# Kernel optimization log

Hardware: AMD Instinct MI355X
Metric: run time of the kernel (lower is better)

The kernel has to match this reference:

```python
import jax, jax.numpy as jnp
import numpy as np

NEG = 0.01  # torch leaky_relu default slope


def conv1d(x, w, pad):
    # x: [B, C, L], w: [O, I, K], stride 1, no bias (as in FC-STGNN extractor)
    return jax.lax.conv_general_dilated(x, w, (1,), [(pad, pad)], dimension_numbers=('NCH', 'OIH', 'NCH'))


def maxpool2(x):
    # MaxPool1d(kernel=2, stride=2, padding=1); torch pads with -inf for max
    return jax.lax.reduce_window(x, -jnp.inf, jax.lax.max, (1, 1, 2), (1, 1, 2), ((0, 0), (0, 0), (1, 1)))


def pos_encoding(n, d):
    # standard sinusoidal PE table, rows 0..n-1 (n <= max_len=5000)
    pos = jnp.arange(n, dtype=jnp.float32)[:, None]
    div = jnp.exp(jnp.arange(0, d, 2, dtype=jnp.float32) * (-float(np.log(10000.0)) / d))
    pe = jnp.zeros((n, d), jnp.float32)
    pe = pe.at[:, 0::2].set(jnp.sin(pos * div))
    pe = pe.at[:, 1::2].set(jnp.cos(pos * div))
    return pe


def mpnn_block(x, gw, gb, bng, bnb, tw, tb):
    # GraphConvpoolMPNN_block_v6 with time_length=1, time_window_size=1, stride=1:
    # one window, decay mask = ones, mean-pool over the size-1 time window is identity.
    bs, two_h, N = x.shape
    X = x.reshape(bs, N, two_h)                                   # (bs*num_windows, num_node*tw, input_dim)
    h = X @ gw + gb                                               # Dot_Graph_Construction mapping
    adj = jnp.einsum('bnd,bmd->bnm', h, h)                        # dot-product adjacency
    eye = jnp.eye(N, dtype=X.dtype)
    adj = jax.nn.leaky_relu(adj - eye * 1e8, NEG)
    adj = jax.nn.softmax(adj, axis=-1) + eye
    Xb = X * bng + bnb                                            # BatchNorm1d eval (running mean 0 / var 1)
    out = jax.nn.leaky_relu(jnp.einsum('bnm,bmd->bnd', adj, Xb) @ tw + tb, NEG)  # MPNN_mk k=1
    return out                                                    # [bs, N, hidden]


def setup_inputs() -> dict:
    key = jax.random.key(0)
    ks = jax.random.split(key, 20)
    bs, D, N = 4, 128, 1024
    H, OUT, KS = 64, 32, 8        # lstmhidden_dim, lstmout_dim, conv_kernel
    HID = 64                      # hidden_dim
    TWOH = 2 * HID
    CONV_OUT = 18
    NCLS = 6
    f32 = jnp.float32
    rn = lambda k, s, sc: jax.random.normal(k, s, f32) * sc
    return {
        'x_enc': rn(ks[0], (bs, D, N), 1.0),
        'x_mark_enc': rn(ks[1], (bs, D, 4), 1.0),
        'x_dec': rn(ks[2], (bs, D // 2, N), 1.0),
        'x_mark_dec': rn(ks[3], (bs, D // 2, 4), 1.0),
        'conv_w1': rn(ks[4], (H, 1, KS), 1.0 / np.sqrt(KS)),
        'bn1_g': jnp.ones((H,), f32), 'bn1_b': jnp.zeros((H,), f32),
        'conv_w2': rn(ks[5], (2 * H, H, KS), 1.0 / np.sqrt(H * KS)),
        'bn2_g': jnp.ones((2 * H,), f32), 'bn2_b': jnp.zeros((2 * H,), f32),
        'conv_w3': rn(ks[6], (OUT, 2 * H, KS), 1.0 / np.sqrt(2 * H * KS)),
        'bn3_g': jnp.ones((OUT,), f32), 'bn3_b': jnp.zeros((OUT,), f32),
        'map2_w': rn(ks[7], (OUT * CONV_OUT, TWOH), 1.0 / np.sqrt(OUT * CONV_OUT)),
        'map2_b': jnp.zeros((TWOH,), f32),
        'map2_bn_g': jnp.ones((TWOH,), f32), 'map2_bn_b': jnp.zeros((TWOH,), f32),
        'g1_w': rn(ks[8], (TWOH, TWOH), 1.0 / np.sqrt(TWOH)), 'g1_b': jnp.zeros((TWOH,), f32),
        'm1_bn_g': jnp.ones((TWOH,), f32), 'm1_bn_b': jnp.zeros((TWOH,), f32),
        't1_w': rn(ks[9], (TWOH, HID), 1.0 / np.sqrt(TWOH)), 't1_b': jnp.zeros((HID,), f32),
        'g2_w': rn(ks[10], (TWOH, TWOH), 1.0 / np.sqrt(TWOH)), 'g2_b': jnp.zeros((TWOH,), f32),
        'm2_bn_g': jnp.ones((TWOH,), f32), 'm2_bn_b': jnp.zeros((TWOH,), f32),
        't2_w': rn(ks[11], (TWOH, HID), 1.0 / np.sqrt(TWOH)), 't2_b': jnp.zeros((HID,), f32),
        'fc1_w': rn(ks[12], (HID * 2 * N, TWOH), 1.0 / np.sqrt(HID * 2 * N)), 'fc1_b': jnp.zeros((TWOH,), f32),
        'fc2_w': rn(ks[13], (TWOH, TWOH), 1.0 / np.sqrt(TWOH)), 'fc2_b': jnp.zeros((TWOH,), f32),
        'fc3_w': rn(ks[14], (TWOH, HID), 1.0 / np.sqrt(TWOH)), 'fc3_b': jnp.zeros((HID,), f32),
        'fc4_w': rn(ks[15], (HID, NCLS), 1.0 / np.sqrt(HID)), 'fc4_b': jnp.zeros((NCLS,), f32),
    }


def reference(x_enc, x_mark_enc, x_dec, x_mark_dec,
              conv_w1, bn1_g, bn1_b, conv_w2, bn2_g, bn2_b, conv_w3, bn3_g, bn3_b,
              map2_w, map2_b, map2_bn_g, map2_bn_b,
              g1_w, g1_b, m1_bn_g, m1_bn_b, t1_w, t1_b,
              g2_w, g2_b, m2_bn_g, m2_bn_b, t2_w, t2_b,
              fc1_w, fc1_b, fc2_w, fc2_b, fc3_w, fc3_b, fc4_w, fc4_b):
    bs, D, N = x_enc.shape
    k = conv_w1.shape[-1]
    # nonlin_map: 1D-CNN feature extractor over each (sample, node) signal
    a = jnp.swapaxes(x_enc.reshape(bs * N, D, 1), 1, 2)           # [bs*N, 1, D]
    a = maxpool2(jax.nn.relu(conv1d(a, conv_w1, k // 2) * bn1_g[None, :, None] + bn1_b[None, :, None]))
    a = maxpool2(jax.nn.relu(conv1d(a, conv_w2, 4) * bn2_g[None, :, None] + bn2_b[None, :, None]))
    a = maxpool2(jax.nn.relu(conv1d(a, conv_w3, 4) * bn3_g[None, :, None] + bn3_b[None, :, None]))
    a = a.reshape(bs * N, -1)                                     # [bs*N, lstmout_dim*conv_out]
    # nonlin_map2: Linear + BatchNorm1d (eval mode affine)
    a = (a @ map2_w + map2_b) * map2_bn_g + map2_bn_b             # [bs*N, 2h]
    two_h = a.shape[-1]
    # positional encoding with the exact reshape/transpose traffic of the torch forward
    x = jnp.swapaxes(a.reshape(bs, N, two_h), 1, 2).reshape(bs * N, two_h)
    x = x + pos_encoding(bs * N, two_h)
    x = jnp.swapaxes(x.reshape(bs, N, two_h), 1, 2)               # [bs, 2h, N]
    # two graph MPNN branches
    o1 = mpnn_block(x, g1_w, g1_b, m1_bn_g, m1_bn_b, t1_w, t1_b)
    o2 = mpnn_block(x, g2_w, g2_b, m2_bn_g, m2_bn_b, t2_w, t2_b)
    f = jnp.concatenate([o1.reshape(bs, -1), o2.reshape(bs, -1)], axis=-1)
    # MLP head
    f = jax.nn.relu(f @ fc1_w + fc1_b)
    f = jax.nn.relu(f @ fc2_w + fc2_b)
    f = jax.nn.relu(f @ fc3_w + fc3_b)
    return f @ fc4_w + fc4_b                                      # [bs, n_class]
```

## Files before the change

### kernel.cpp

```cpp
#include <hip/hip_runtime.h>
#include <hip/hip_bf16.h>
#include <math.h>

#define NEG 0.01f
__device__ __forceinline__ float lrelu(float v){ return v > 0.f ? v : NEG*v; }
__device__ __forceinline__ float frelu(float v){ return v > 0.f ? v : 0.f; }

typedef __attribute__((ext_vector_type(8))) short bf16x8;
typedef __attribute__((ext_vector_type(4))) float f32x4;

__device__ __forceinline__ unsigned short f2bf(float x){
    unsigned int u = __float_as_uint(x);
    unsigned int r = (u + 0x7FFFu + ((u>>16)&1u)) >> 16;
    return (unsigned short)r;
}
__device__ __forceinline__ float bf2f(unsigned short h){
    return __uint_as_float(((unsigned int)h) << 16);
}
__device__ __forceinline__ unsigned short F2B(float x){
    __hip_bfloat16 h = __float2bfloat16(x);
    return *reinterpret_cast<unsigned short*>(&h);
}

__global__ __launch_bounds__(256) void k_prep(const float* __restrict__ w2, const float* __restrict__ w3,
    const float* __restrict__ m2w, const float* __restrict__ t1w, const float* __restrict__ t2w,
    unsigned short* __restrict__ w2s, unsigned short* __restrict__ w3s, unsigned short* __restrict__ m2wbT,
    unsigned short* __restrict__ twThi, unsigned short* __restrict__ twTlo)
{
    int gid = blockIdx.x*256 + threadIdx.x;
    if (gid < 73728) {
        int j = gid / 576, f = gid % 576;
        m2wbT[gid] = f2bf(m2w[f*128 + j]);
    }
    if (gid < 65536) {
        int jj = gid & 7, q = (gid>>3)&3, o = (gid>>5)&127, ks = (gid>>12)&1, k = gid>>13;
        int c = ks*32 + q*8 + jj;
        w2s[gid] = f2bf(w2[o*512 + c*8 + k]);
    }
    if (gid < 32768) {
        int jj = gid & 7, q = (gid>>3)&3, o = (gid>>5)&31, ks = (gid>>10)&3, k = gid>>12;
        int c = ks*32 + q*8 + jj;
        w3s[gid] = f2bf(w3[o*1024 + c*8 + k]);
    }
    if (gid < 16384) {
        int d = gid & 127, e = (gid>>7)&63, br = gid>>13;
        float x = (br ? t2w : t1w)[d*64 + e];
        unsigned short hh = f2bf(x);
        twThi[gid] = hh;
        twTlo[gid] = f2bf(x - bf2f(hh));
    }
}

__global__ __launch_bounds__(256) void k_conv(
    const float* __restrict__ xenc,
    const float* __restrict__ w1, const float* __restrict__ g1, const float* __restrict__ b1,
    const unsigned short* __restrict__ w2s, const float* __restrict__ g2, const float* __restrict__ b2,
    const unsigned short* __restrict__ w3s, const float* __restrict__ g3, const float* __restrict__ b3,
    unsigned short* __restrict__ aflatG)
{
    __shared__ __align__(16) unsigned char smraw[22208];
    float* sigp = (float*)smraw;
    unsigned short* p1T = (unsigned short*)(smraw + 576);
    unsigned short* p2T = (unsigned short*)(smraw + 10304);
    unsigned short* astage = (unsigned short*)(smraw + 21056);

    const int t = threadIdx.x;
    const int s = blockIdx.x;

    {
        unsigned int* zz = (unsigned int*)(smraw + 576);
        for (int i = t; i < 5120; i += 256) zz[i] = 0u;
        if (t < 144) sigp[t] = 0.f;
    }
    __syncthreads();
    if (t < 128) sigp[4 + t] = xenc[(size_t)s*128 + t];
    __syncthreads();

    {
        const int c = t & 63, qg = t >> 6;
        float wr[8];
        #pragma unroll
        for (int k = 0; k < 8; ++k) wr[k] = w1[c*8 + k];
        const float g = g1[c], b = b1[c];
        const int qs = qg*17;
        float win[9];
        {
            int base = 2*qs - 1;
            #pragma unroll
            for (int x = 0; x < 9; ++x) win[x] = (base + x >= 0) ? sigp[base + x] : 0.f;
        }
        #pragma unroll
        for (int j = 0; j < 17; ++j) {
            int q = qs + j;
            float s0 = 0.f, s1 = 0.f;
            #pragma unroll
            for (int k = 0; k < 8; ++k) { s0 += win[k]*wr[k]; s1 += win[k+1]*wr[k]; }
            float v = frelu(s1*g + b);
            if (q > 0) v = fmaxf(v, frelu(s0*g + b));
            if (q < 65) {
                int row = q + 4;
                p1T[row*64 + (((c>>3) ^ (row&7))<<3) + (c&7)] = F2B(v);
            }
            #pragma unroll
            for (int x = 0; x < 7; ++x) win[x] = win[x+2];
            win[7] = sigp[2*q + 8];
            win[8] = sigp[2*q + 9];
        }
    }
    __syncthreads();

    {
        const int wv = t >> 6, l = t & 63, lg = l >> 4, lr = l & 15;
        const int pbase = ((lr & 7) << 1) + (lr >> 3) - 1;
        f32x4 acc[2][5] = {};
        for (int k = 0; k < 8; ++k) {
            for (int ks = 0; ks < 2; ++ks) {
                bf16x8 af[2];
                #pragma unroll
                for (int oi = 0; oi < 2; ++oi) {
                    int o = (wv*2 + oi)*16 + lr;
                    af[oi] = *(const bf16x8*)(w2s + ((((k*2 + ks)*128 + o)*4 + lg)<<3));
                }
                const int q = ks*4 + lg;
                #pragma unroll
                for (int nt = 0; nt < 5; ++nt) {
                    int row = nt*16 + pbase + k; row = row > 75 ? 75 : row;
                    bf16x8 bfv = *(const bf16x8*)(p1T + row*64 + ((q ^ (row&7))<<3));
                    acc[0][nt] = __builtin_amdgcn_mfma_f32_16x16x32_bf16(af[0], bfv, acc[0][nt], 0,0,0);
                    acc[1][nt] = __builtin_amdgcn_mfma_f32_16x16x32_bf16(af[1], bfv, acc[1][nt], 0,0,0);
                }
            }
        }
        float ga[2][4], ba[2][4];
        #pragma unroll
        for (int oi = 0; oi < 2; ++oi)
            #pragma unroll
            for (int r = 0; r < 4; ++r) {
                int o = (wv*2 + oi)*16 + lg*4 + r;
                ga[oi][r] = g2[o]; ba[oi][r] = b2[o];
            }
        #pragma unroll
        for (int oi = 0; oi < 2; ++oi)
            #pragma unroll
            for (int nt = 0; nt < 5; ++nt) {
                int p = nt*16 + pbase;
                bool valid = (p >= 0) && (p <= 65);
                float vv[4];
                #pragma unroll
                for (int r = 0; r < 4; ++r) {
                    float v = frelu(acc[oi][nt][r]*ga[oi][r] + ba[oi][r]);
                    vv[r] = valid ? v : -3.0e38f;
                }
                float pv[4];
                #pragma unroll
                for (int r = 0; r < 4; ++r) pv[r] = fmaxf(vv[r], __shfl_xor(vv[r], 8));
                int q = nt*8 + (lr & 7);
                if ((lr >> 3) == 0 && q < 34) {
                    int row2 = q + 4;
                    int o0 = (wv*2 + oi)*16 + lg*4;
                    uint2 pk;
                    pk.x = (unsigned int)F2B(pv[0]) | ((unsigned int)F2B(pv[1]) << 16);
                    pk.y = (unsigned int)F2B(pv[2]) | ((unsigned int)F2B(pv[3]) << 16);
                    *(uint2*)&p2T[row2*128 + (((o0>>3) ^ (row2&15))<<3) + (o0&7)] = pk;
                }
            }
    }
    __syncthreads();

    {
        const int wv = t >> 6, l = t & 63, lg = l >> 4, lr = l & 15;
        const int ot = wv & 1, ntb = (wv >> 1) * 2;
        const int ncnt = (wv < 2) ? 2 : 1;
        const int pbase = ((lr & 7) << 1) + (lr >> 3) - 1;
        f32x4 acc[2] = {};
        for (int k = 0; k < 8; ++k) {
            for (int ks = 0; ks < 4; ++ks) {
                int o = ot*16 + lr;
                bf16x8 af = *(const bf16x8*)(w3s + ((((k*4 + ks)*32 + o)*4 + lg)<<3));
                const int q = ks*4 + lg;
                #pragma unroll
                for (int ni = 0; ni < 2; ++ni) {
                    if (ni < ncnt) {
                        int row = (ntb + ni)*16 + pbase + k; row = row > 41 ? 41 : row;
                        bf16x8 bfv = *(const bf16x8*)(p2T + row*128 + ((q ^ (row&15))<<3));
                        acc[ni] = __builtin_amdgcn_mfma_f32_16x16x32_bf16(af, bfv, acc[ni], 0,0,0);
                    }
                }
            }
        }
        float g3v[4], b3v[4];
        #pragma unroll
        for (int r = 0; r < 4; ++r) {
            int o = ot*16 + lg*4 + r;
            g3v[r] = g3[o]; b3v[r] = b3[o];
        }
        #pragma unroll
        for (int ni = 0; ni < 2; ++ni) if (ni < ncnt) {
            int p = (ntb + ni)*16 + pbase;
            bool valid = (p >= 0) && (p <= 34);
            float vv[4];
            #pragma unroll
            for (int r = 0; r < 4; ++r) {
                float v = frelu(acc[ni][r]*g3v[r] + b3v[r]);
                vv[r] = valid ? v : -3.0e38f;
            }
            float pv[4];
            #pragma unroll
            for (int r = 0; r < 4; ++r) pv[r] = fmaxf(vv[r], __shfl_xor(vv[r], 8));
            int q = (ntb + ni)*8 + (lr & 7);
            if ((lr >> 3) == 0 && q < 18) {
                #pragma unroll
                for (int r = 0; r < 4; ++r)
                    astage[(ot*16 + lg*4 + r)*18 + q] = F2B(pv[r]);
            }
        }
    }
    __syncthreads();

    for (int idx = t; idx < 576; idx += 256)
        aflatG[(size_t)s*576 + idx] = astage[idx];
}

__global__ __launch_bounds__(256) void k_map2(const unsigned short* __restrict__ aflatG,
    const unsigned short* __restrict__ m2wbT,
    const float* __restrict__ m2b, const float* __restrict__ m2g, const float* __restrict__ m2bb,
    float* __restrict__ a2)
{
    const int t = threadIdx.x, wv = t>>6, l = t&63, lg = l>>4, lr = l&15;
    const int s0 = blockIdx.x*64;
    f32x4 acc[8] = {};
    for (int ks = 0; ks < 18; ++ks) {
        bf16x8 a = *(const bf16x8*)(aflatG + (size_t)(s0 + wv*16 + lr)*576 + ks*32 + lg*8);
        #pragma unroll
        for (int nt = 0; nt < 8; ++nt) {
            bf16x8 b = *(const bf16x8*)(m2wbT + (size_t)(nt*16 + lr)*576 + ks*32 + lg*8);
            acc[nt] = __builtin_amdgcn_mfma_f32_16x16x32_bf16(a, b, acc[nt], 0,0,0);
        }
    }
    #pragma unroll
    for (int nt = 0; nt < 8; ++nt)
        #pragma unroll
        for (int r = 0; r < 4; ++r) {
            int s2 = s0 + wv*16 + lg*4 + r;
            int j = nt*16 + lr;
            a2[(size_t)s2*128 + j] = (acc[nt][r] + m2b[j]) * m2g[j] + m2bb[j];
        }
}

__global__ __launch_bounds__(256) void k_buildx(const float* __restrict__ a2, float* __restrict__ X)
{
    __shared__ double dvt[64];
    const int t = threadIdx.x;
    if (t < 64) dvt[t] = exp((double)(2*t) * (-9.210340371976184/128.0));
    __syncthreads();
    int e = blockIdx.x*256 + t;
    int b = e >> 17;
    int r = e & 131071;
    int i = r >> 7, d = r & 127;
    int row = b*1024 + (d & 7)*128 + (i >> 3);
    int col = (i & 7)*16 + (d >> 3);
    float v = a2[row*128 + col];
    int per = b*1024 + (i & 7)*128 + d;
    int pc  = i >> 3;
    double ang = (double)per * dvt[pc >> 1];
    const double TWO_PI = 6.283185307179586476925287;
    double kk = floor(ang * (1.0/TWO_PI) + 0.5);
    float red = (float)(ang - kk * TWO_PI);
    float pe = (pc & 1) ? __cosf(red) : __sinf(red);
    X[e] = v + pe;
}

__global__ __launch_bounds__(256) void k_hmat(const float* __restrict__ X,
    const float* __restrict__ g1w, const float* __restrict__ g1b,
    const float* __restrict__ g2w, const float* __restrict__ g2b,
    unsigned short* __restrict__ Hbhi1, unsigned short* __restrict__ Hblo1,
    unsigned short* __restrict__ Hbhi2, unsigned short* __restrict__ Hblo2)
{
    const int br = blockIdx.y;
    const float* gw = br ? g2w : g1w;
    const float* gb = br ? g2b : g1b;
    unsigned short* Hh = br ? Hbhi2 : Hbhi1;
    unsigned short* Hl = br ? Hblo2 : Hblo1;
    int e = blockIdx.x*256 + threadIdx.x;
    int srow = e >> 7, j = e & 127;
    const float* xr = X + (size_t)srow*128;
    float acc = gb[j];
    for (int k = 0; k < 128; ++k) acc += xr[k] * gw[k*128 + j];
    unsigned short hh = f2bf(acc);
    Hh[e] = hh;
    Hl[e] = f2bf(acc - bf2f(hh));
}

__global__ __launch_bounds__(256) void k_scores(
    const unsigned short* __restrict__ Hbhi1, const unsigned short* __restrict__ Hblo1,
    const unsigned short* __restrict__ Hbhi2, const unsigned short* __restrict__ Hblo2,
    float* __restrict__ S1, float* __restrict__ S2)
{
    __shared__ __align__(16) unsigned short HiH[64*64];
    __shared__ __align__(16) unsigned short HiL[64*64];
    __shared__ __align__(16) unsigned short HjH[64*64];
    __shared__ __align__(16) unsigned short HjL[64*64];
    const int z = blockIdx.z;
    const int b = z & 3, br = z >> 2;
    const unsigned short* Hbhi = br ? Hbhi2 : Hbhi1;
    const unsigned short* Hblo = br ? Hblo2 : Hblo1;
    float* S = br ? S2 : S1;
    const int i0 = blockIdx.y * 64, j0 = blockIdx.x * 64;
    const int t = threadIdx.x;
    const int w = t >> 6, l = t & 63, lr = l & 15, h = l >> 4;
    const size_t hb = (size_t)b * 1024 * 128;

    f32x4 acc[4] = {};
    for (int kh = 0; kh < 2; ++kh) {
        __syncthreads();
        #pragma unroll
        for (int it = 0; it < 4; ++it) {
            int g = it*256 + t;
            int mat = g >> 9;
            int gg = g & 511;
            int row = gg >> 3, ch = gg & 7;
            int base0 = mat ? j0 : i0;
            size_t src = hb + (size_t)(base0 + row)*128 + kh*64 + ch*8;
            uint4 vh = *(const uint4*)(Hbhi + src);
            uint4 vl = *(const uint4*)(Hblo + src);
            int sw = ch ^ (row & 7);
            unsigned short* dh = (mat ? HjH : HiH) + row*64 + sw*8;
            unsigned short* dl = (mat ? HjL : HiL) + row*64 + sw*8;
            *(uint4*)dh = vh;
            *(uint4*)dl = vl;
        }
        __syncthreads();
        #pragma unroll
        for (int kc = 0; kc < 2; ++kc) {
            int swA = (((kc*4 + h) ^ (lr & 7)) << 3);
            bf16x8 ah = *(const bf16x8*)&HiH[(w*16 + lr)*64 + swA];
            bf16x8 al = *(const bf16x8*)&HiL[(w*16 + lr)*64 + swA];
            #pragma unroll
            for (int jt = 0; jt < 4; ++jt) {
                bf16x8 bh = *(const bf16x8*)&HjH[(jt*16 + lr)*64 + swA];
                bf16x8 bl = *(const bf16x8*)&HjL[(jt*16 + lr)*64 + swA];
                acc[jt] = __builtin_amdgcn_mfma_f32_16x16x32_bf16(ah, bh, acc[jt], 0,0,0);
                acc[jt] = __builtin_amdgcn_mfma_f32_16x16x32_bf16(ah, bl, acc[jt], 0,0,0);
                acc[jt] = __builtin_amdgcn_mfma_f32_16x16x32_bf16(al, bh, acc[jt], 0,0,0);
            }
        }
    }
    float* Sb = S + (size_t)b*1024*1024;
    #pragma unroll
    for (int jt = 0; jt < 4; ++jt) {
        #pragma unroll
        for (int r = 0; r < 4; ++r) {
            int i = i0 + w*16 + h*4 + r;
            int j = j0 + jt*16 + lr;
            float x = acc[jt][r];
            if (i == j) x -= 1e8f;
            Sb[(size_t)i*1024 + j] = lrelu(x);
        }
    }
}

__global__ __launch_bounds__(256) void k_rowstat(const float* __restrict__ S1, const float* __restrict__ S2,
                                                 float* __restrict__ mrow, float* __restrict__ linv)
{
    __shared__ float red[256];
    const int y = blockIdx.y, i = blockIdx.x, t = threadIdx.x;
    const int b = y & 3, br = y >> 2;
    const float* row = (br ? S2 : S1) + (size_t)b*1024*1024 + (size_t)i*1024;
    float4 v = *(const float4*)&row[t*4];
    float mx = fmaxf(fmaxf(v.x,v.y), fmaxf(v.z,v.w));
    red[t] = mx; __syncthreads();
    for (int s2 = 128; s2 > 0; s2 >>= 1) { if (t < s2) red[t] = fmaxf(red[t], red[t+s2]); __syncthreads(); }
    mx = red[0]; __syncthreads();
    float e = (__expf(v.x-mx) + __expf(v.y-mx)) + (__expf(v.z-mx) + __expf(v.w-mx));
    red[t] = e; __syncthreads();
    for (int s2 = 128; s2 > 0; s2 >>= 1) { if (t < s2) red[t] += red[t+s2]; __syncthreads(); }
    if (t == 0) { mrow[y*1024 + i] = mx; linv[y*1024 + i] = 1.f / red[0]; }
}

__global__ __launch_bounds__(256) void k_xbbt(const float* __restrict__ X,
    const float* __restrict__ bng1, const float* __restrict__ bnb1,
    const float* __restrict__ bng2, const float* __restrict__ bnb2,
    unsigned short* __restrict__ XbbThi, unsigned short* __restrict__ XbbTlo)
{
    __shared__ float Xl[64][132];
    const int t = threadIdx.x;
    const int j0 = blockIdx.x*64, b = blockIdx.y, br = blockIdx.z;
    {
        int r2 = t >> 2, dseg = (t & 3)*32;
        const float* src = X + ((size_t)(b*1024 + j0 + r2))*128 + dseg;
        #pragma unroll
        for (int q = 0; q < 8; ++q) {
            float4 v = *(const float4*)(src + q*4);
            Xl[r2][dseg + q*4 + 0] = v.x;
            Xl[r2][dseg + q*4 + 1] = v.y;
            Xl[r2][dseg + q*4 + 2] = v.z;
            Xl[r2][dseg + q*4 + 3] = v.w;
        }
    }
    __syncthreads();
    const int d = t >> 1, seg = t & 1;
    const float g  = (br ? bng2 : bng1)[d];
    const float bb = (br ? bnb2 : bnb1)[d];
    unsigned short* dsth = XbbThi + (size_t)br*524288 + ((size_t)(b*128 + d))*1024 + j0 + seg*32;
    unsigned short* dstl = XbbTlo + (size_t)br*524288 + ((size_t)(b*128 + d))*1024 + j0 + seg*32;
    #pragma unroll
    for (int g8 = 0; g8 < 4; ++g8) {
        unsigned int hu[4], lu[4];
        #pragma unroll
        for (int q = 0; q < 4; ++q) {
            float v0 = Xl[seg*32 + g8*8 + 2*q    ][d]*g + bb;
            float v1 = Xl[seg*32 + g8*8 + 2*q + 1][d]*g + bb;
            unsigned short h0 = f2bf(v0), h1 = f2bf(v1);
            hu[q] = (unsigned int)h0 | ((unsigned int)h1 << 16);
            lu[q] = (unsigned int)f2bf(v0 - bf2f(h0)) | ((unsigned int)f2bf(v1 - bf2f(h1)) << 16);
        }
        *(uint4*)(dsth + g8*8) = make_uint4(hu[0],hu[1],hu[2],hu[3]);
        *(uint4*)(dstl + g8*8) = make_uint4(lu[0],lu[1],lu[2],lu[3]);
    }
}

__global__ __launch_bounds__(256) void k_pvmm(
    const float* __restrict__ S1, const float* __restrict__ S2, const float* __restrict__ X,
    const float* __restrict__ bng1, const float* __restrict__ bnb1,
    const float* __restrict__ bng2, const float* __restrict__ bnb2,
    const float* __restrict__ mrow, const float* __restrict__ linv,
    const unsigned short* __restrict__ XbbThi, const unsigned short* __restrict__ XbbTlo,
    unsigned short* __restrict__ Phi, unsigned short* __restrict__ Plo)
{
    __shared__ __align__(16) unsigned short ElH[16*64];
    __shared__ __align__(16) unsigned short ElL[16*64];
    const int t = threadIdx.x;
    const int w = t >> 6, l = t & 63, lr = l & 15, h = l >> 4;
    const int i0 = blockIdx.x * 16;
    const int b = blockIdx.y;
    const int br = blockIdx.z;
    const float* S = br ? S2 : S1;
    const float* bng = br ? bng2 : bng1;
    const float* bnb = br ? bnb2 : bnb1;
    const float* mr = mrow + br*4096 + b*1024;
    const float* lv = linv + br*4096 + b*1024;
    const unsigned short* Bh = XbbThi + (size_t)br*524288 + (size_t)b*131072;
    const unsigned short* Bl = XbbTlo + (size_t)br*524288 + (size_t)b*131072;

    const int srow = t >> 4, jseg = t & 15;
    const float mi = mr[i0 + srow];
    const int j0s = jseg*4;
    const int eoff = srow*64 + (((j0s>>3) ^ (srow&7))<<3) + (j0s&7);

    f32x4 acc[2] = {};
    for (int ch = 0; ch < 16; ++ch) {
        const int jb = ch*64;
        __syncthreads();
        {
            float4 sv = *(const float4*)(S + ((size_t)(b*1024 + i0 + srow))*1024 + jb + j0s);
            float e0 = __expf(sv.x - mi), e1 = __expf(sv.y - mi);
            float e2 = __expf(sv.z - mi), e3 = __expf(sv.w - mi);
            unsigned short h0 = f2bf(e0), h1 = f2bf(e1), h2 = f2bf(e2), h3 = f2bf(e3);
            uint2 vh, vl;
            vh.x = (unsigned int)h0 | ((unsigned int)h1 << 16);
            vh.y = (unsigned int)h2 | ((unsigned int)h3 << 16);
            vl.x = (unsigned int)f2bf(e0 - bf2f(h0)) | ((unsigned int)f2bf(e1 - bf2f(h1)) << 16);
            vl.y = (unsigned int)f2bf(e2 - bf2f(h2)) | ((unsigned int)f2bf(e3 - bf2f(h3)) << 16);
            *(uint2*)(ElH + eoff) = vh;
            *(uint2*)(ElL + eoff) = vl;
        }
        __syncthreads();
        #pragma unroll
        for (int kc = 0; kc < 2; ++kc) {
            int swA = (((kc*4 + h) ^ (lr & 7)) << 3);
            bf16x8 ah = *(const bf16x8*)&ElH[lr*64 + swA];
            bf16x8 al = *(const bf16x8*)&ElL[lr*64 + swA];
            #pragma unroll
            for (int n2 = 0; n2 < 2; ++n2) {
                int nt = w*2 + n2;
                size_t boff = (size_t)(nt*16 + lr)*1024 + jb + kc*32 + h*8;
                bf16x8 bh = *(const bf16x8*)(Bh + boff);
                bf16x8 bl = *(const bf16x8*)(Bl + boff);
                acc[n2] = __builtin_amdgcn_mfma_f32_16x16x32_bf16(ah, bh, acc[n2], 0,0,0);
                acc[n2] = __builtin_amdgcn_mfma_f32_16x16x32_bf16(ah, bl, acc[n2], 0,0,0);
                acc[n2] = __builtin_amdgcn_mfma_f32_16x16x32_bf16(al, bh, acc[n2], 0,0,0);
            }
        }
    }
    #pragma unroll
    for (int r = 0; r < 4; ++r) {
        int i = i0 + h*4 + r;
        float inv = lv[i];
        #pragma unroll
        for (int n2 = 0; n2 < 2; ++n2) {
            int d = (w*2 + n2)*16 + lr;
            float xv = X[((size_t)(b*1024 + i))*128 + d] * bng[d] + bnb[d];
            float pv = acc[n2][r]*inv + xv;
            size_t off = ((size_t)(br*4096 + b*1024 + i))*128 + d;
            unsigned short hh = f2bf(pv);
            Phi[off] = hh;
            Plo[off] = f2bf(pv - bf2f(hh));
        }
    }
}

__global__ __launch_bounds__(256) void k_tprojmm(
    const unsigned short* __restrict__ Phi, const unsigned short* __restrict__ Plo,
    const unsigned short* __restrict__ twThi, const unsigned short* __restrict__ twTlo,
    const float* __restrict__ t1b, const float* __restrict__ t2b,
    float* __restrict__ O)
{
    const int t = threadIdx.x, w = t>>6, l = t&63, lr = l&15, h = l>>4;
    const int r0 = blockIdx.x*16;
    const int br = r0 >> 12;
    f32x4 acc = {};
    #pragma unroll
    for (int kc = 0; kc < 4; ++kc) {
        size_t aoff = (size_t)(r0 + lr)*128 + kc*32 + h*8;
        bf16x8 ah = *(const bf16x8*)(Phi + aoff);
        bf16x8 al = *(const bf16x8*)(Plo + aoff);
        size_t boff = (size_t)(br*64 + w*16 + lr)*128 + kc*32 + h*8;
        bf16x8 bh = *(const bf16x8*)(twThi + boff);
        bf16x8 bl = *(const bf16x8*)(twTlo + boff);
        acc = __builtin_amdgcn_mfma_f32_16x16x32_bf16(ah, bh, acc, 0,0,0);
        acc = __builtin_amdgcn_mfma_f32_16x16x32_bf16(ah, bl, acc, 0,0,0);
        acc = __builtin_amdgcn_mfma_f32_16x16x32_bf16(al, bh, acc, 0,0,0);
    }
    const float* tb = br ? t2b : t1b;
    float tbe = tb[w*16 + lr];
    int rowLocal0 = r0 & 4095;
    #pragma unroll
    for (int r = 0; r < 4; ++r) {
        int row = rowLocal0 + h*4 + r;
        O[(size_t)br*262144 + (size_t)row*64 + w*16 + lr] = lrelu(acc[r] + tbe);
    }
}

__global__ __launch_bounds__(256) void k_pv(const float* __restrict__ S, const float* __restrict__ X,
                                            const float* __restrict__ bng, const float* __restrict__ bnb,
                                            const float* __restrict__ mrowG, const float* __restrict__ linvG,
                                            float* __restrict__ P)
{
    __shared__ __align__(16) float Sl[16*65];
    __shared__ __align__(16) float Xl[64*132];
    const int b = blockIdx.y, i0 = blockIdx.x*16, t = threadIdx.x;
    const int il = t >> 4, dg = t & 15;
    const int sj = t & 63, sil = t >> 6;
    const int xd = t & 127, xj = t >> 7;
    const float bg = bng[xd], bb = bnb[xd];
    float mr[4];
    #pragma unroll
    for (int m2 = 0; m2 < 4; ++m2) mr[m2] = mrowG[b*1024 + i0 + sil*4 + m2];
    float acc[8] = {};
    const float* Sb = S + (size_t)b*1024*1024;
    const float* Xb = X + (size_t)b*1024*128;
    for (int c = 0; c < 16; ++c) {
        int jb = c*64;
        __syncthreads();
        #pragma unroll
        for (int m2 = 0; m2 < 4; ++m2) {
            int r2 = sil*4 + m2;
            Sl[r2*65 + sj] = __expf(Sb[(size_t)(i0+r2)*1024 + jb + sj] - mr[m2]);
        }
        #pragma unroll
        for (int m2 = 0; m2 < 32; ++m2) {
            int jc = xj + 2*m2;
            Xl[jc*132 + xd] = Xb[(size_t)(jb+jc)*128 + xd] * bg + bb;
        }
        __syncthreads();
        for (int jc = 0; jc < 64; ++jc) {
            float sv = Sl[il*65 + jc];
            float4 x0 = *(const float4*)&Xl[jc*132 + dg*8];
            float4 x1 = *(const float4*)&Xl[jc*132 + dg*8 + 4];
            acc[0] += sv*x0.x; acc[1] += sv*x0.y; acc[2] += sv*x0.z; acc[3] += sv*x0.w;
            acc[4] += sv*x1.x; acc[5] += sv*x1.y; acc[6] += sv*x1.z; acc[7] += sv*x1.w;
        }
    }
    int i = i0 + il;
    float inv = linvG[b*1024 + i];
    const float* xr = Xb + (size_t)i*128 + dg*8;
    float* pr = P + (size_t)(b*1024 + i)*128 + dg*8;
    #pragma unroll
    for (int z = 0; z < 8; ++z) {
        float xv = xr[z] * bng[dg*8+z] + bnb[dg*8+z];
        pr[z] = acc[z]*inv + xv;
    }
}

__global__ __launch_bounds__(256) void k_tproj(const float* __restrict__ P, const float* __restrict__ tw,
                                               const float* __restrict__ tb, float* __restrict__ O)
{
    int idx = blockIdx.x*256 + threadIdx.x;
    int srow = idx >> 6, e = idx & 63;
    const float* pr = P + (size_t)srow*128;
    float acc = tb[e];
    for (int d = 0; d < 128; ++d) acc += pr[d] * tw[d*64 + e];
    O[idx] = lrelu(acc);
}

__global__ __launch_bounds__(256) void k_fc1(const float* __restrict__ O1, const float* __restrict__ O2,
                                             const float* __restrict__ w, float* __restrict__ pbuf)
{
    __shared__ float red[4*512];
    const int t = threadIdx.x;
    const int wv = t >> 6, l = t & 63;
    const int gwid = blockIdx.x*4 + wv;
    float acc[4][2] = {};
    int base = gwid*64;
    for (int tt = 0; tt < 64; ++tt) {
        int row = base + tt;
        float2 wvv = *(const float2*)&w[(size_t)row*128 + l*2];
        #pragma unroll
        for (int b = 0; b < 4; ++b) {
            float fb = (row < 65536) ? O1[b*65536 + row] : O2[b*65536 + row - 65536];
            acc[b][0] += fb * wvv.x;
            acc[b][1] += fb * wvv.y;
        }
    }
    #pragma unroll
    for (int b = 0; b < 4; ++b) {
        red[wv*512 + b*128 + l*2]   = acc[b][0];
        red[wv*512 + b*128 + l*2+1] = acc[b][1];
    }
    __syncthreads();
    for (int rep = 0; rep < 2; ++rep) {
        int col = rep*256 + t;
        pbuf[(size_t)blockIdx.x*512 + col] = red[col] + red[512+col] + red[1024+col] + red[1536+col];
    }
}

__global__ __launch_bounds__(256) void k_red(const float* __restrict__ pbuf, float* __restrict__ pbuf2)
{
    int col = blockIdx.x*8 + (threadIdx.x >> 5);
    int lane = threadIdx.x & 31;
    float acc = 0.f;
    for (int it = 0; it < 16; ++it)
        acc += pbuf[(size_t)(lane + it*32)*512 + col];
    #pragma unroll
    for (int s2 = 16; s2 >= 1; s2 >>= 1) acc += __shfl_xor(acc, s2, 32);
    if (lane == 0) pbuf2[col] = acc;
}

__global__ __launch_bounds__(256) void k_head2(const float* __restrict__ pbuf2,
    const float* __restrict__ fc1b, const float* __restrict__ fc2w, const float* __restrict__ fc2b,
    const float* __restrict__ fc3w, const float* __restrict__ fc3b,
    const float* __restrict__ fc4w, const float* __restrict__ fc4b,
    float* __restrict__ out)
{
    __shared__ float r1[512], r2[512], r3[256];
    const int t = threadIdx.x;
    for (int rep = 0; rep < 2; ++rep) {
        int idx = rep*256 + t;
        r1[idx] = frelu(pbuf2[idx] + fc1b[idx & 127]);
    }
    __syncthreads();
    for (int rep = 0; rep < 2; ++rep) {
        int idx = rep*256 + t;
        int b = idx >> 7, j = idx & 127;
        float acc = fc2b[j];
        for (int k = 0; k < 128; ++k) acc += r1[b*128+k]*fc2w[k*128+j];
        r2[idx] = frelu(acc);
    }
    __syncthreads();
    {
        int b = t >> 6, e2 = t & 63;
        float acc = fc3b[e2];
        for (int k = 0; k < 128; ++k) acc += r2[b*128+k]*fc3w[k*64+e2];
        r3[t] = frelu(acc);
    }
    __syncthreads();
    if (t < 24) {
        int b = t/6, c = t%6;
        float acc = fc4b[c];
        for (int k = 0; k < 64; ++k) acc += r3[b*64+k]*fc4w[k*6+c];
        out[b*6+c] = acc;
    }
}

extern "C" void kernel_launch(void* const* d_in, const int* in_sizes, int n_in,
                              void* d_out, int out_size, void* d_ws, size_t ws_size,
                              hipStream_t stream)
{
    (void)in_sizes; (void)n_in; (void)out_size;
    const float* xenc = (const float*)d_in[0];
    const float* w1   = (const float*)d_in[4];
    const float* g1   = (const float*)d_in[5];
    const float* b1   = (const float*)d_in[6];
    const float* w2   = (const float*)d_in[7];
    const float* g2   = (const float*)d_in[8];
    const float* b2   = (const float*)d_in[9];
    const float* w3   = (const float*)d_in[10];
    const float* g3   = (const float*)d_in[11];
    const float* b3   = (const float*)d_in[12];
    const float* m2w  = (const float*)d_in[13];
    const float* m2b  = (const float*)d_in[14];
    const float* m2g  = (const float*)d_in[15];
    const float* m2bb = (const float*)d_in[16];
    const float* g1w  = (const float*)d_in[17];
    const float* g1b  = (const float*)d_in[18];
    const float* m1g  = (const float*)d_in[19];
    const float* m1b  = (const float*)d_in[20];
    const float* t1w  = (const float*)d_in[21];
    const float* t1b  = (const float*)d_in[22];
    const float* g2w  = (const float*)d_in[23];
    const float* g2bv = (const float*)d_in[24];
    const float* mm2g = (const float*)d_in[25];
    const float* mm2b = (const float*)d_in[26];
    const float* t2w  = (const float*)d_in[27];
    const float* t2b  = (const float*)d_in[28];
    const float* fc1w = (const float*)d_in[29];
    const float* fc1b = (const float*)d_in[30];
    const float* fc2w = (const float*)d_in[31];
    const float* fc2b = (const float*)d_in[32];
    const float* fc3w = (const float*)d_in[33];
    const float* fc3b = (const float*)d_in[34];
    const float* fc4w = (const float*)d_in[35];
    const float* fc4b = (const float*)d_in[36];

    char* ws = (char*)d_ws;
    float* a2   = (float*)(ws);
    float* X    = (float*)(ws + (2u<<20));
    unsigned short* Hbhi1 = (unsigned short*)(ws + (4u<<20));
    unsigned short* Hblo1 = (unsigned short*)(ws + (5u<<20));
    unsigned short* Hbhi2 = (unsigned short*)(ws);
    unsigned short* Hblo2 = (unsigned short*)(ws + (1u<<20));
    float* S1   = (float*)(ws + (6u<<20));
    unsigned short* aflatG = (unsigned short*)(ws + (6u<<20));
    unsigned short* w2s    = (unsigned short*)(ws + (6u<<20) + 5242880);
    unsigned short* w3s    = (unsigned short*)(ws + (6u<<20) + 5242880 + 131072);
    unsigned short* m2wbT  = (unsigned short*)(ws + (6u<<20) + 5242880 + 196608);
    float* pbuf2 = (float*)(ws + (6u<<20));

    if (ws_size >= ((size_t)49 << 20)) {
        float* S2   = (float*)(ws + (22u<<20));
        unsigned short* Phi = (unsigned short*)(ws + (38u<<20));
        unsigned short* Plo = (unsigned short*)(ws + (40u<<20));
        float* O    = (float*)(ws + (42u<<20));
        float* pbuf = (float*)(ws + (44u<<20));
        float* mrow = (float*)(ws + (44u<<20));
        float* linv = (float*)(ws + (44u<<20) + 65536);
        unsigned short* twThi = (unsigned short*)(ws + (44u<<20) + 131072);
        unsigned short* twTlo = (unsigned short*)(ws + (44u<<20) + 196608);
        unsigned short* XbbThi = (unsigned short*)(ws + (45u<<20));
        unsigned short* XbbTlo = (unsigned short*)(ws + (47u<<20));
        float* O1 = O;
        float* O2 = O + 262144;

        k_prep<<<288, 256, 0, stream>>>(w2, w3, m2w, t1w, t2w, w2s, w3s, m2wbT, twThi, twTlo);
        k_conv<<<4096, 256, 0, stream>>>(xenc, w1,g1,b1, w2s,g2,b2, w3s,g3,b3, aflatG);
        k_map2<<<64, 256, 0, stream>>>(aflatG, m2wbT, m2b, m2g, m2bb, a2);
        k_buildx<<<2048, 256, 0, stream>>>(a2, X);
        k_hmat<<<dim3(2048,2), 256, 0, stream>>>(X, g1w, g1b, g2w, g2bv,
                                                 Hbhi1, Hblo1, Hbhi2, Hblo2);
        k_xbbt<<<dim3(16,4,2), 256, 0, stream>>>(X, m1g, m1b, mm2g, mm2b, XbbThi, XbbTlo);
        k_scores <<<dim3(16,16,8), 256, 0, stream>>>(Hbhi1, Hblo1, Hbhi2, Hblo2, S1, S2);
        k_rowstat<<<dim3(1024,8), 256, 0, stream>>>(S1, S2, mrow, linv);
        k_pvmm<<<dim3(64,4,2), 256, 0, stream>>>(S1, S2, X, m1g, m1b, mm2g, mm2b,
                                                 mrow, linv, XbbThi, XbbTlo, Phi, Plo);
        k_tprojmm<<<512, 256, 0, stream>>>(Phi, Plo, twThi, twTlo, t1b, t2b, O);
        k_fc1 <<<512, 256, 0, stream>>>(O1, O2, fc1w, pbuf);
        k_red <<<64, 256, 0, stream>>>(pbuf, pbuf2);
        k_head2<<<1, 256, 0, stream>>>(pbuf2, fc1b, fc2w, fc2b, fc3w, fc3b, fc4w, fc4b, (float*)d_out);
    } else {
        float* P    = (float*)(ws + (22u<<20));
        float* O1   = (float*)(ws + (24u<<20));
        float* O2   = (float*)(ws + (25u<<20));
        float* pbuf = (float*)(ws + (26u<<20));
        float* mrow = (float*)(ws + (26u<<20));
        float* linv = (float*)(ws + (26u<<20) + 65536);
        unsigned short* twThi = (unsigned short*)(ws + (26u<<20) + 131072);
        unsigned short* twTlo = (unsigned short*)(ws + (26u<<20) + 196608);

        k_prep<<<288, 256, 0, stream>>>(w2, w3, m2w, t1w, t2w, w2s, w3s, m2wbT, twThi, twTlo);
        k_conv<<<4096, 256, 0, stream>>>(xenc, w1,g1,b1, w2s,g2,b2, w3s,g3,b3, aflatG);
        k_map2<<<64, 256, 0, stream>>>(aflatG, m2wbT, m2b, m2g, m2bb, a2);
        k_buildx<<<2048, 256, 0, stream>>>(a2, X);
        k_hmat<<<dim3(2048,2), 256, 0, stream>>>(X, g1w, g1b, g2w, g2bv,
                                                 Hbhi1, Hblo1, Hbhi2, Hblo2);
        k_scores <<<dim3(16,16,4), 256, 0, stream>>>(Hbhi1, Hblo1, Hbhi1, Hblo1, S1, S1);
        k_rowstat<<<dim3(1024,4), 256, 0, stream>>>(S1, S1, mrow, linv);
        k_pv     <<<dim3(64,4), 256, 0, stream>>>(S1, X, m1g, m1b, mrow, linv, P);
        k_tproj  <<<1024, 256, 0, stream>>>(P, t1w, t1b, O1);
        k_scores <<<dim3(16,16,4), 256, 0, stream>>>(Hbhi2, Hblo2, Hbhi2, Hblo2, S1, S1);
        k_rowstat<<<dim3(1024,4), 256, 0, stream>>>(S1, S1, mrow, linv);
        k_pv     <<<dim3(64,4), 256, 0, stream>>>(S1, X, mm2g, mm2b, mrow, linv, P);
        k_tproj  <<<1024, 256, 0, stream>>>(P, t2w, t2b, O2);
        k_fc1 <<<512, 256, 0, stream>>>(O1, O2, fc1w, pbuf);
        k_red <<<64, 256, 0, stream>>>(pbuf, pbuf2);
        k_head2<<<1, 256, 0, stream>>>(pbuf2, fc1b, fc2w, fc2b, fc3w, fc3b, fc4w, fc4b, (float*)d_out);
    }
}
```

Baseline: 262.6 us.

## Fuse scores, row softmax stats and PV matmul into one flash-style attention kernel

Replaces the separate score, row-statistics and PV kernels with a single k_attn kernel. It computes the HH^T scores with split-bf16 MFMA, applies the diagonal mask and leaky ReLU, and keeps an online softmax per row. Each wave handles a quarter of the key range, and the per-wave partial results are merged through shared memory. This removes the round trips of the 2x4x1024x1024 fp32 score matrices through global memory and two kernel launches. In exchange the attention work runs on only 512 blocks with heavy register use, and the score products are recomputed inside the fused loop.

```diff
diff --git a/kernel.cpp b/kernel.cpp
--- a/kernel.cpp
+++ b/kernel.cpp
@@ -419,83 +419,226 @@
     }
 }
 
-__global__ __launch_bounds__(256) void k_pvmm(
-    const float* __restrict__ S1, const float* __restrict__ S2, const float* __restrict__ X,
+__global__ __launch_bounds__(256) void k_attn(
+    const unsigned short* __restrict__ Hbhi1, const unsigned short* __restrict__ Hblo1,
+    const unsigned short* __restrict__ Hbhi2, const unsigned short* __restrict__ Hblo2,
+    const float* __restrict__ X,
     const float* __restrict__ bng1, const float* __restrict__ bnb1,
     const float* __restrict__ bng2, const float* __restrict__ bnb2,
-    const float* __restrict__ mrow, const float* __restrict__ linv,
     const unsigned short* __restrict__ XbbThi, const unsigned short* __restrict__ XbbTlo,
     unsigned short* __restrict__ Phi, unsigned short* __restrict__ Plo)
 {
-    __shared__ __align__(16) unsigned short ElH[16*64];
-    __shared__ __align__(16) unsigned short ElL[16*64];
-    const int t = threadIdx.x;
-    const int w = t >> 6, l = t & 63, lr = l & 15, h = l >> 4;
+    __shared__ __align__(16) unsigned char lbuf[33280];
+    const int t = threadIdx.x, w = t >> 6, l = t & 63, lr = l & 15, h = l >> 4;
+    unsigned short* ElH = (unsigned short*)(lbuf + w*4096);
+    unsigned short* ElL = (unsigned short*)(lbuf + w*4096 + 2048);
+    float* Pred = (float*)lbuf;
+    float* mW = (float*)(lbuf + 32768);
+    float* lW = (float*)(lbuf + 32768 + 256);
+
     const int i0 = blockIdx.x * 16;
-    const int b = blockIdx.y;
+    const int b  = blockIdx.y;
     const int br = blockIdx.z;
-    const float* S = br ? S2 : S1;
+    const unsigned short* Hh = br ? Hbhi2 : Hbhi1;
+    const unsigned short* Hl = br ? Hblo2 : Hblo1;
+    const unsigned short* Bh = XbbThi + (size_t)br*524288 + (size_t)b*131072;
+    const unsigned short* Bl = XbbTlo + (size_t)br*524288 + (size_t)b*131072;
     const float* bng = br ? bng2 : bng1;
     const float* bnb = br ? bnb2 : bnb1;
-    const float* mr = mrow + br*4096 + b*1024;
-    const float* lv = linv + br*4096 + b*1024;
-    const unsigned short* Bh = XbbThi + (size_t)br*524288 + (size_t)b*131072;
-    const unsigned short* Bl = XbbTlo + (size_t)br*524288 + (size_t)b*131072;
-
-    const int srow = t >> 4, jseg = t & 15;
-    const float mi = mr[i0 + srow];
-    const int j0s = jseg*4;
-    const int eoff = srow*64 + (((j0s>>3) ^ (srow&7))<<3) + (j0s&7);
-
-    f32x4 acc[2] = {};
-    for (int ch = 0; ch < 16; ++ch) {
-        const int jb = ch*64;
-        __syncthreads();
-        {
-            float4 sv = *(const float4*)(S + ((size_t)(b*1024 + i0 + srow))*1024 + jb + j0s);
-            float e0 = __expf(sv.x - mi), e1 = __expf(sv.y - mi);
-            float e2 = __expf(sv.z - mi), e3 = __expf(sv.w - mi);
-            unsigned short h0 = f2bf(e0), h1 = f2bf(e1), h2 = f2bf(e2), h3 = f2bf(e3);
-            uint2 vh, vl;
-            vh.x = (unsigned int)h0 | ((unsigned int)h1 << 16);
-            vh.y = (unsigned int)h2 | ((unsigned int)h3 << 16);
-            vl.x = (unsigned int)f2bf(e0 - bf2f(h0)) | ((unsigned int)f2bf(e1 - bf2f(h1)) << 16);
-            vl.y = (unsigned int)f2bf(e2 - bf2f(h2)) | ((unsigned int)f2bf(e3 - bf2f(h3)) << 16);
-            *(uint2*)(ElH + eoff) = vh;
-            *(uint2*)(ElL + eoff) = vl;
-        }
-        __syncthreads();
+    const size_t hb = (size_t)b * 1024 * 128;
+
+    bf16x8 ahi[4], alo[4];
+    #pragma unroll
+    for (int kc = 0; kc < 4; ++kc) {
+        size_t aoff = hb + (size_t)(i0 + lr)*128 + kc*32 + h*8;
+        ahi[kc] = *(const bf16x8*)(Hh + aoff);
+        alo[kc] = *(const bf16x8*)(Hl + aoff);
+    }
+
+    float m[4] = {-3.0e38f,-3.0e38f,-3.0e38f,-3.0e38f};
+    float lsum[4] = {};
+    f32x4 pacc[8] = {};
+
+    for (int ch = 0; ch < 4; ++ch) {
+        const int jbase = w*256 + ch*64;
+        float sv[4][4];
+        float cmax[4] = {-3.0e38f,-3.0e38f,-3.0e38f,-3.0e38f};
+        #pragma unroll
+        for (int jt = 0; jt < 4; ++jt) {
+            f32x4 c = {};
+            #pragma unroll
+            for (int kc = 0; kc < 4; ++kc) {
+                size_t boff = hb + (size_t)(jbase + jt*16 + lr)*128 + kc*32 + h*8;
+                bf16x8 bh_ = *(const bf16x8*)(Hh + boff);
+                bf16x8 bl_ = *(const bf16x8*)(Hl + boff);
+                c = __builtin_amdgcn_mfma_f32_16x16x32_bf16(ahi[kc], bh_, c, 0,0,0);
+                c = __builtin_amdgcn_mfma_f32_16x16x32_bf16(ahi[kc], bl_, c, 0,0,0);
+                c = __builtin_amdgcn_mfma_f32_16x16x32_bf16(alo[kc], bh_, c, 0,0,0);
+            }
+            #pragma unroll
+            for (int r = 0; r < 4; ++r) {
+                float x = c[r];
+                int ig = i0 + h*4 + r;
+                int jg = jbase + jt*16 + lr;
+                if (ig == jg) x -= 1e8f;
+                x = lrelu(x);
+                sv[jt][r] = x;
+                cmax[r] = fmaxf(cmax[r], x);
+            }
+        }
+        #pragma unroll
+        for (int r = 0; r < 4; ++r) {
+            cmax[r] = fmaxf(cmax[r], __shfl_xor(cmax[r], 1));
+            cmax[r] = fmaxf(cmax[r], __shfl_xor(cmax[r], 2));
+            cmax[r] = fmaxf(cmax[r], __shfl_xor(cmax[r], 4));
+            cmax[r] = fmaxf(cmax[r], __shfl_xor(cmax[r], 8));
+        }
+        float scale[4];
+        #pragma unroll
+        for (int r = 0; r < 4; ++r) {
+            float mn = fmaxf(m[r], cmax[r]);
+            scale[r] = __expf(m[r] - mn);
+            m[r] = mn;
+        }
+        float csum[4] = {};
+        #pragma unroll
+        for (int jt = 0; jt < 4; ++jt)
+            #pragma unroll
+            for (int r = 0; r < 4; ++r) {
+                float e = __expf(sv[jt][r] - m[r]);
+                csum[r] += e;
+                unsigned short eh = f2bf(e);
+                unsigned short el = f2bf(e - bf2f(eh));
+                int ip = h*4 + r;
+                int jp = jt*16 + lr;
+                int addr = ip*64 + (((jp>>3) ^ (ip&7))<<3) + (jp&7);
+                ElH[addr] = eh;
+                ElL[addr] = el;
+            }
+        #pragma unroll
+        for (int r = 0; r < 4; ++r) {
+            csum[r] += __shfl_xor(csum[r], 1);
+            csum[r] += __shfl_xor(csum[r], 2);
+            csum[r] += __shfl_xor(csum[r], 4);
+            csum[r] += __shfl_xor(csum[r], 8);
+            lsum[r] = lsum[r]*scale[r] + csum[r];
+        }
+        #pragma unroll
+        for (int dt = 0; dt < 8; ++dt)
+            #pragma unroll
+            for (int r = 0; r < 4; ++r) pacc[dt][r] *= scale[r];
         #pragma unroll
         for (int kc = 0; kc < 2; ++kc) {
             int swA = (((kc*4 + h) ^ (lr & 7)) << 3);
-            bf16x8 ah = *(const bf16x8*)&ElH[lr*64 + swA];
-            bf16x8 al = *(const bf16x8*)&ElL[lr*64 + swA];
-            #pragma unroll
-            for (int n2 = 0; n2 < 2; ++n2) {
-                int nt = w*2 + n2;
-                size_t boff = (size_t)(nt*16 + lr)*1024 + jb + kc*32 + h*8;
-                bf16x8 bh = *(const bf16x8*)(Bh + boff);
-                bf16x8 bl = *(const bf16x8*)(Bl + boff);
-                acc[n2] = __builtin_amdgcn_mfma_f32_16x16x32_bf16(ah, bh, acc[n2], 0,0,0);
-                acc[n2] = __builtin_amdgcn_mfma_f32_16x16x32_bf16(ah, bl, acc[n2], 0,0,0);
-                acc[n2] = __builtin_amdgcn_mfma_f32_16x16x32_bf16(al, bh, acc[n2], 0,0,0);
-            }
-        }
-    }
-    #pragma unroll
-    for (int r = 0; r < 4; ++r) {
-        int i = i0 + h*4 + r;
-        float inv = lv[i];
-        #pragma unroll
-        for (int n2 = 0; n2 < 2; ++n2) {
-            int d = (w*2 + n2)*16 + lr;
-            float xv = X[((size_t)(b*1024 + i))*128 + d] * bng[d] + bnb[d];
-            float pv = acc[n2][r]*inv + xv;
-            size_t off = ((size_t)(br*4096 + b*1024 + i))*128 + d;
-            unsigned short hh = f2bf(pv);
-            Phi[off] = hh;
-            Plo[off] = f2bf(pv - bf2f(hh));
-        }
+            bf16x8 eh8 = *(const bf16x8*)&ElH[lr*64 + swA];
+            bf16x8 el8 = *(const bf16x8*)&ElL[lr*64 + swA];
+            #pragma unroll
+            for (int dt = 0; dt < 8; ++dt) {
+                size_t boff = (size_t)(dt*16 + lr)*1024 + jbase + kc*32 + h*8;
+                bf16x8 bh_ = *(const bf16x8*)(Bh + boff);
+                bf16x8 bl_ = *(const bf16x8*)(Bl + boff);
+                pacc[dt] = __builtin_amdgcn_mfma_f32_16x16x32_bf16(eh8, bh_, pacc[dt], 0,0,0);
+                pacc[dt] = __builtin_amdgcn_mfma_f32_16x16x32_bf16(eh8, bl_, pacc[dt], 0,0,0);
+                pacc[dt] = __builtin_amdgcn_mfma_f32_16x16x32_bf16(el8, bh_, pacc[dt], 0,0,0);
+            }
+        }
+    }
+
+    __syncthreads();
+    #pragma unroll
+    for (int dt = 0; dt < 8; ++dt)
+        #pragma unroll
+        for (int r = 0; r < 4; ++r)
+            Pred[w*2048 + (h*4 + r)*128 + dt*16 + lr] = pacc[dt][r];
+    if (lr == 0) {
+        #pragma unroll
+        for (int r = 0; r < 4; ++r) {
+            mW[w*16 + h*4 + r] = m[r];
+            lW[w*16 + h*4 + r] = lsum[r];
+        }
+    }
+    __syncthreads();
+
+    {
+        int i = t >> 4, d0 = (t & 15) * 8;
+        float m0 = mW[i], m1 = mW[16 + i], m2 = mW[32 + i], m3 = mW[48 + i];
+        float ms = fmaxf(fmaxf(m0, m1), fmaxf(m2, m3));
+        float e0 = __expf(m0 - ms), e1 = __expf(m1 - ms);
+        float e2 = __expf(m2 - ms), e3 = __expf(m3 - ms);
+        float ls = lW[i]*e0 + lW[16+i]*e1 + lW[32+i]*e2 + lW[48+i]*e3;
+        float inv = 1.f / ls;
+        unsigned int ph[4], pl[4];
+        #pragma unroll
+        for (int q2 = 0; q2 < 4; ++q2) {
+            unsigned short hh0, hh1, ll0, ll1;
+            #pragma unroll
+            for (int half = 0; half < 2; ++half) {
+                int d = d0 + 2*q2 + half;
+                float P = Pred[i*128 + d]*e0 + Pred[2048 + i*128 + d]*e1
+                        + Pred[4096 + i*128 + d]*e2 + Pred[6144 + i*128 + d]*e3;
+                float xv = X[((size_t)(b*1024 + i0 + i))*128 + d] * bng[d] + bnb[d];
+                float pv = P*inv + xv;
+                unsigned short hh = f2bf(pv);
+                unsigned short ll = f2bf(pv - bf2f(hh));
+                if (half == 0) { hh0 = hh; ll0 = ll; } else { hh1 = hh; ll1 = ll; }
+            }
+            ph[q2] = (unsigned int)hh0 | ((unsigned int)hh1 << 16);
+            pl[q2] = (unsigned int)ll0 | ((unsigned int)ll1 << 16);
+        }
+        size_t off = ((size_t)(br*4096 + b*1024 + i0 + i))*128 + d0;
+        *(uint4*)(Phi + off) = make_uint4(ph[0],ph[1],ph[2],ph[3]);
+        *(uint4*)(Plo + off) = make_uint4(pl[0],pl[1],pl[2],pl[3]);
+    }
+}
+
+__global__ __launch_bounds__(256) void k_pv(const float* __restrict__ S, const float* __restrict__ X,
+                                            const float* __restrict__ bng, const float* __restrict__ bnb,
+                                            const float* __restrict__ mrowG, const float* __restrict__ linvG,
+                                            float* __restrict__ P)
+{
+    __shared__ __align__(16) float Sl[16*65];
+    __shared__ __align__(16) float Xl[64*132];
+    const int b = blockIdx.y, i0 = blockIdx.x*16, t = threadIdx.x;
+    const int il = t >> 4, dg = t & 15;
+    const int sj = t & 63, sil = t >> 6;
+    const int xd = t & 127, xj = t >> 7;
+    const float bg = bng[xd], bb = bnb[xd];
+    float mr[4];
+    #pragma unroll
+    for (int m2 = 0; m2 < 4; ++m2) mr[m2] = mrowG[b*1024 + i0 + sil*4 + m2];
+    float acc[8] = {};
+    const float* Sb = S + (size_t)b*1024*1024;
+    const float* Xb = X + (size_t)b*1024*128;
+    for (int c = 0; c < 16; ++c) {
+        int jb = c*64;
+        __syncthreads();
+        #pragma unroll
+        for (int m2 = 0; m2 < 4; ++m2) {
+            int r2 = sil*4 + m2;
+            Sl[r2*65 + sj] = __expf(Sb[(size_t)(i0+r2)*1024 + jb + sj] - mr[m2]);
+        }
+        #pragma unroll
+        for (int m2 = 0; m2 < 32; ++m2) {
+            int jc = xj + 2*m2;
+            Xl[jc*132 + xd] = Xb[(size_t)(jb+jc)*128 + xd] * bg + bb;
+        }
+        __syncthreads();
+        for (int jc = 0; jc < 64; ++jc) {
+            float sv = Sl[il*65 + jc];
+            float4 x0 = *(const float4*)&Xl[jc*132 + dg*8];
+            float4 x1 = *(const float4*)&Xl[jc*132 + dg*8 + 4];
+            acc[0] += sv*x0.x; acc[1] += sv*x0.y; acc[2] += sv*x0.z; acc[3] += sv*x0.w;
+            acc[4] += sv*x1.x; acc[5] += sv*x1.y; acc[6] += sv*x1.z; acc[7] += sv*x1.w;
+        }
+    }
+    int i = i0 + il;
+    float inv = linvG[b*1024 + i];
+    const float* xr = Xb + (size_t)i*128 + dg*8;
+    float* pr = P + (size_t)(b*1024 + i)*128 + dg*8;
+    #pragma unroll
+    for (int z = 0; z < 8; ++z) {
+        float xv = xr[z] * bng[dg*8+z] + bnb[dg*8+z];
+        pr[z] = acc[z]*inv + xv;
     }
 }
 
@@ -528,57 +671,6 @@
     for (int r = 0; r < 4; ++r) {
         int row = rowLocal0 + h*4 + r;
         O[(size_t)br*262144 + (size_t)row*64 + w*16 + lr] = lrelu(acc[r] + tbe);
-    }
-}
-
-__global__ __launch_bounds__(256) void k_pv(const float* __restrict__ S, const float* __restrict__ X,
-                                            const float* __restrict__ bng, const float* __restrict__ bnb,
-                                            const float* __restrict__ mrowG, const float* __restrict__ linvG,
-                                            float* __restrict__ P)
-{
-    __shared__ __align__(16) float Sl[16*65];
-    __shared__ __align__(16) float Xl[64*132];
-    const int b = blockIdx.y, i0 = blockIdx.x*16, t = threadIdx.x;
-    const int il = t >> 4, dg = t & 15;
-    const int sj = t & 63, sil = t >> 6;
-    const int xd = t & 127, xj = t >> 7;
-    const float bg = bng[xd], bb = bnb[xd];
-    float mr[4];
-    #pragma unroll
-    for (int m2 = 0; m2 < 4; ++m2) mr[m2] = mrowG[b*1024 + i0 + sil*4 + m2];
-    float acc[8] = {};
-    const float* Sb = S + (size_t)b*1024*1024;
-    const float* Xb = X + (size_t)b*1024*128;
-    for (int c = 0; c < 16; ++c) {
-        int jb = c*64;
-        __syncthreads();
-        #pragma unroll
-        for (int m2 = 0; m2 < 4; ++m2) {
-            int r2 = sil*4 + m2;
-            Sl[r2*65 + sj] = __expf(Sb[(size_t)(i0+r2)*1024 + jb + sj] - mr[m2]);
-        }
-        #pragma unroll
-        for (int m2 = 0; m2 < 32; ++m2) {
-            int jc = xj + 2*m2;
-            Xl[jc*132 + xd] = Xb[(size_t)(jb+jc)*128 + xd] * bg + bb;
-        }
-        __syncthreads();
-        for (int jc = 0; jc < 64; ++jc) {
-            float sv = Sl[il*65 + jc];
-            float4 x0 = *(const float4*)&Xl[jc*132 + dg*8];
-            float4 x1 = *(const float4*)&Xl[jc*132 + dg*8 + 4];
-            acc[0] += sv*x0.x; acc[1] += sv*x0.y; acc[2] += sv*x0.z; acc[3] += sv*x0.w;
-            acc[4] += sv*x1.x; acc[5] += sv*x1.y; acc[6] += sv*x1.z; acc[7] += sv*x1.w;
-        }
-    }
-    int i = i0 + il;
-    float inv = linvG[b*1024 + i];
-    const float* xr = Xb + (size_t)i*128 + dg*8;
-    float* pr = P + (size_t)(b*1024 + i)*128 + dg*8;
-    #pragma unroll
-    for (int z = 0; z < 8; ++z) {
-        float xv = xr[z] * bng[dg*8+z] + bnb[dg*8+z];
-        pr[z] = acc[z]*inv + xv;
     }
 }
 
@@ -727,13 +819,10 @@
     float* pbuf2 = (float*)(ws + (6u<<20));
 
     if (ws_size >= ((size_t)49 << 20)) {
-        float* S2   = (float*)(ws + (22u<<20));
         unsigned short* Phi = (unsigned short*)(ws + (38u<<20));
         unsigned short* Plo = (unsigned short*)(ws + (40u<<20));
         float* O    = (float*)(ws + (42u<<20));
         float* pbuf = (float*)(ws + (44u<<20));
-        float* mrow = (float*)(ws + (44u<<20));
-        float* linv = (float*)(ws + (44u<<20) + 65536);
         unsigned short* twThi = (unsigned short*)(ws + (44u<<20) + 131072);
         unsigned short* twTlo = (unsigned short*)(ws + (44u<<20) + 196608);
         unsigned short* XbbThi = (unsigned short*)(ws + (45u<<20));
@@ -748,10 +837,9 @@
         k_hmat<<<dim3(2048,2), 256, 0, stream>>>(X, g1w, g1b, g2w, g2bv,
                                                  Hbhi1, Hblo1, Hbhi2, Hblo2);
         k_xbbt<<<dim3(16,4,2), 256, 0, stream>>>(X, m1g, m1b, mm2g, mm2b, XbbThi, XbbTlo);
-        k_scores <<<dim3(16,16,8), 256, 0, stream>>>(Hbhi1, Hblo1, Hbhi2, Hblo2, S1, S2);
-        k_rowstat<<<dim3(1024,8), 256, 0, stream>>>(S1, S2, mrow, linv);
-        k_pvmm<<<dim3(64,4,2), 256, 0, stream>>>(S1, S2, X, m1g, m1b, mm2g, mm2b,
-                                                 mrow, linv, XbbThi, XbbTlo, Phi, Plo);
+        k_attn<<<dim3(64,4,2), 256, 0, stream>>>(Hbhi1, Hblo1, Hbhi2, Hblo2, X,
+                                                 m1g, m1b, mm2g, mm2b,
+                                                 XbbThi, XbbTlo, Phi, Plo);
         k_tprojmm<<<512, 256, 0, stream>>>(Phi, Plo, twThi, twTlo, t1b, t2b, O);
         k_fc1 <<<512, 256, 0, stream>>>(O1, O2, fc1w, pbuf);
         k_red <<<64, 256, 0, stream>>>(pbuf, pbuf2);
```

New measurement: 260.5 us. Within noise of the previous version (-0.8%).
